# Kernel optimization log

Hardware: AMD Instinct MI355X
Metric: run time of the kernel (lower is better)

## Reference

```python
import math
import jax
import jax.numpy as jnp
import numpy as np

B, N = 64, 64
R = N * (N - 1)
DIST_THRESH = 0.35


def _pair_indices(n):
    # edge e = i*(n-1) + j - (j > i): row-major over i, ascending j skipping j == i
    ii = np.repeat(np.arange(n), n - 1)
    jm = np.tile(np.arange(n), (n, 1))
    jj = jm[~np.eye(n, dtype=bool)].reshape(-1)
    return ii, jj


def _rot_basis(a):
    # a: [..., 1] angle -> [..., 2, 2] rotation basis rows [cos,sin],[cos(a+pi/2),sin(a+pi/2)]
    first = jnp.concatenate([jnp.cos(a), jnp.sin(a)], axis=-1)
    second = jnp.concatenate([jnp.cos(a + math.pi / 2), jnp.sin(a + math.pi / 2)], axis=-1)
    return jnp.stack([first, second], axis=-2)


def setup_inputs() -> dict:
    ks = jax.random.split(jax.random.key(0), 8)
    nrm = lambda k, shape, s=1.0: (jax.random.normal(k, shape) * s).astype(jnp.float32)
    return dict(
        objects_state=jax.random.uniform(ks[0], (B, N, 8), dtype=jnp.float32),
        objects_shape=nrm(ks[1], (B, N, 10)),
        relation_info=nrm(ks[2], (B, R, 3)),
        s_mean=jnp.zeros((8,), jnp.float32), s_std=jnp.ones((8,), jnp.float32),
        sh_mean=jnp.zeros((10,), jnp.float32), sh_std=jnp.ones((10,), jnp.float32),
        v_mean=jnp.zeros((3,), jnp.float32), v_std=jnp.ones((3,), jnp.float32),
        W1=nrm(ks[3], (32, 256), 32 ** -0.5), b1=jnp.zeros((256,), jnp.float32),
        W2=nrm(ks[4], (256, 128), 256 ** -0.5), b2=jnp.zeros((128,), jnp.float32),
        W3=nrm(ks[5], (141, 256), 141 ** -0.5), b3=jnp.zeros((256,), jnp.float32),
        W4=nrm(ks[6], (256, 3), 256 ** -0.5), b4=jnp.zeros((3,), jnp.float32),
    )


def reference(objects_state, objects_shape, relation_info, s_mean, s_std, sh_mean, sh_std,
              v_mean, v_std, W1, b1, W2, b2, W3, b3, W4, b4):
    n = objects_state.shape[1]
    ii, jj = _pair_indices(n)

    # ---- pre_proces: distance-threshold edge build into dense one-hot matrices ----
    pos = objects_state[:, :, 0:2]
    dist = jnp.sqrt(jnp.sum((pos[:, :, None, :] - pos[:, None, :, :]) ** 2, axis=-1))
    # torch: where(dist<0.35, dist, 0).nonzero() -> keeps dist<0.35 AND dist != 0 (drops self-edges)
    mask = ((dist < DIST_THRESH) & (dist != 0.0)).astype(jnp.float32)
    mask_flat = mask[:, ii, jj]  # [B, R]
    eye = jnp.eye(n, dtype=jnp.float32)
    receiver_relations = mask_flat[:, :, None] * eye[ii][None]  # [B, R, N]
    sender_relations = mask_flat[:, :, None] * eye[jj][None]    # [B, R, N]

    data_state = (objects_state - s_mean) / s_std
    data_shape = (objects_shape - sh_mean) / sh_std

    senders_state = jnp.einsum('brn,bnd->brd', sender_relations, data_state)
    receivers_state = jnp.einsum('brn,bnd->brd', receiver_relations, data_state)
    senders_shape = jnp.einsum('brn,bnd->brd', sender_relations, data_shape)
    receivers_shape = jnp.einsum('brn,bnd->brd', receiver_relations, data_shape)

    basis = _rot_basis(receivers_state[:, :, 2:3])  # [B, R, 2, 2]
    diff_state = senders_state - receivers_state
    temp = jnp.stack([diff_state[:, :, 0:2], diff_state[:, :, 3:5], senders_state[:, :, 6:8]], axis=-1)  # [B,R,2,3]
    tfed = jnp.einsum('brij,brjk->brik', basis, temp)  # [B,R,2,3]
    angle_diff = diff_state[:, :, 2:3]
    diff_feat = jnp.concatenate([
        tfed[:, :, :, 0], tfed[:, :, :, 1], tfed[:, :, :, 2],
        jnp.sin(2 * angle_diff), jnp.cos(2 * angle_diff),
        diff_state[:, :, 5:6],
    ], axis=-1)  # [B, R, 9]
    rel_data = jnp.concatenate([relation_info, diff_feat, receivers_shape, senders_shape], axis=-1)  # [B,R,32]

    obj_basis = _rot_basis(data_state[:, :, 2:3])  # [B, N, 2, 2]
    obj_vel_tfed = jnp.einsum('bnij,bnj->bni', obj_basis, data_state[:, :, 3:5])
    obj_data = jnp.concatenate([obj_vel_tfed, data_state[:, :, 5:6], data_shape], axis=-1)  # [B,N,13]

    # ---- interaction-network Net ----
    effects = jax.nn.relu(rel_data @ W1 + b1) @ W2 + b2  # [B, R, 128]
    agg = jnp.einsum('brn,bre->bne', receiver_relations, effects)  # [B, N, 128]
    out_vel = jax.nn.relu(jnp.concatenate([obj_data, agg], axis=-1) @ W3 + b3) @ W4 + b4  # [B,N,3]

    # ---- post_proces ----
    angles = objects_state[:, 1:, 2:3]
    pred = out_vel[:, 1:, :] * v_std + v_mean  # inv_transform_vel
    basis_back = _rot_basis(-angles)
    vel_back = jnp.einsum('bnij,bnj->bni', basis_back, pred[:, :, :2])
    x_dot = jnp.concatenate([vel_back, pred[:, :, 2:]], axis=-1)  # [B, N-1, 3]

    tp = np.eye(6, dtype=np.float32)
    tp[3:, 3:] = 0.0
    tq = np.zeros((3, 6), dtype=np.float32)
    for i in range(3):
        tq[i, i] = 1.0
        tq[i, 3 + i] = 1.0
    x_next = objects_state[:, 1:, :6] @ jnp.asarray(tp) + x_dot @ jnp.asarray(tq)
    return x_next  # [B, N-1, 6]
```

## Files before the change

kernel.cpp:

```cpp
#include <hip/hip_runtime.h>
#include <math.h>

#define BB 64
#define NN 64
#define NM1 63
#define RR (NN*(NN-1))

#define WS1_OFF 0
#define WS2_OFF 16384
#define WS3_OFF 81920

typedef short bf16x8 __attribute__((ext_vector_type(8)));
typedef float f32x4 __attribute__((ext_vector_type(4)));
union U4 { uint4 u; bf16x8 b; };

__device__ inline unsigned int f2bf(float f) {
    unsigned int u = __float_as_uint(f);
    return (u + 0x7FFFu + ((u >> 16) & 1u)) >> 16;
}
__device__ inline unsigned int pack2(float a, float b) {
    return f2bf(a) | (f2bf(b) << 16);
}

__global__ __launch_bounds__(256) void prep_kernel(
    const float* __restrict__ W1, const float* __restrict__ W2,
    const float* __restrict__ W3, unsigned char* __restrict__ ws)
{
    const int t = threadIdx.x;
    const int u = blockIdx.x*4 + (t >> 6), l = t & 63;
    const int col16 = l & 15, quad = l >> 4;
    float v[8];
    uint4* dst;
    if (u < 16) {
        const int nt = u, col = nt*16 + col16;
        #pragma unroll
        for (int j = 0; j < 8; ++j) {
            const int k = quad*8 + j;
            const int orig = k < 12 ? k : (k < 22 ? k+10 : k-10);
            v[j] = W1[orig*256 + col];
        }
        dst = (uint4*)(ws + WS1_OFF) + (nt*64 + l);
    } else if (u < 80) {
        const int w = u-16, nt = w >> 3, kc = w & 7, col = nt*16 + col16;
        #pragma unroll
        for (int j = 0; j < 8; ++j)
            v[j] = W2[(size_t)(kc*32 + quad*8 + j)*128 + col];
        dst = (uint4*)(ws + WS2_OFF) + ((nt*8 + kc)*64 + l);
    } else {
        const int w = u-80, nt = w/5, kc = w - nt*5, col = nt*16 + col16;
        #pragma unroll
        for (int j = 0; j < 8; ++j) {
            const int k = kc*32 + quad*8 + j;
            v[j] = (k < 141) ? W3[(size_t)k*256 + col] : 0.f;
        }
        dst = (uint4*)(ws + WS3_OFF) + ((nt*5 + kc)*64 + l);
    }
    uint4 o;
    o.x = pack2(v[0], v[1]); o.y = pack2(v[2], v[3]);
    o.z = pack2(v[4], v[5]); o.w = pack2(v[6], v[7]);
    *dst = o;
}

__global__ __launch_bounds__(512) void main_kernel(
    const float* __restrict__ objects_state,
    const float* __restrict__ objects_shape,
    const float* __restrict__ relation_info,
    const float* __restrict__ s_mean, const float* __restrict__ s_std,
    const float* __restrict__ sh_mean, const float* __restrict__ sh_std,
    const float* __restrict__ v_mean, const float* __restrict__ v_std,
    const float* __restrict__ b1, const float* __restrict__ b2,
    const float* __restrict__ b3,
    const float* __restrict__ W4, const float* __restrict__ b4,
    const unsigned char* __restrict__ ws,
    float* __restrict__ out)
{
    __shared__ __align__(16) float P[64][29];
    __shared__ __align__(16) unsigned int relb_w[8*64*16];
    __shared__ __align__(16) unsigned short s_h[16*264];
    __shared__ __align__(16) unsigned short s_q[16*168];
    __shared__ int   s_cntg[8];
    __shared__ float s_red[8][16][3];
    __shared__ float s_outv[16][3];

    const int b  = blockIdx.x >> 3;
    const int nb = (blockIdx.x & 7) * 8;
    const int t  = threadIdx.x;
    const int wv = t >> 6, lane = t & 63, col16 = lane & 15, quad = lane >> 4;

    U4 bu0, bu1;
    {
        const uint4* w1f = (const uint4*)(ws + WS1_OFF);
        bu0.u = w1f[(wv*2+0)*64 + lane];
        bu1.u = w1f[(wv*2+1)*64 + lane];
    }
    const float b10 = b1[(wv*2+0)*16 + col16];
    const float b11 = b1[(wv*2+1)*16 + col16];

    float ri0 = 0.f, ri1 = 0.f, ri2 = 0.f;
    if (lane < 63) {
        const float* rp = relation_info
            + ((size_t)b*RR + (size_t)(nb + wv)*NM1 + lane)*3;
        ri0 = rp[0]; ri1 = rp[1]; ri2 = rp[2];
    }

    float e_vs0=0.f,e_vs1=0.f,e_vs2=0.f,e_vm0=0.f,e_vm1=0.f,e_vm2=0.f,e_b4=0.f;
    if (t < 48) {
        e_vs0 = v_std[0]; e_vs1 = v_std[1]; e_vs2 = v_std[2];
        e_vm0 = v_mean[0]; e_vm1 = v_mean[1]; e_vm2 = v_mean[2];
        e_b4  = b4[t % 3];
    }

    {
        uint4 z = make_uint4(0,0,0,0);
        uint4* relb4 = (uint4*)relb_w;
        #pragma unroll
        for (int r = 0; r < 4; ++r) relb4[r*512 + t] = z;
        if (t < 336) ((uint4*)s_q)[t] = z;
        if (t < 64) {
            const int n = b*64 + t;
            const float4* sp4 = (const float4*)(objects_state + (size_t)n*8);
            const float4 sA = sp4[0], sB = sp4[1];
            float st[8] = {sA.x, sA.y, sA.z, sA.w, sB.x, sB.y, sB.z, sB.w};
            const float2* hp2 = (const float2*)(objects_shape + (size_t)n*10);
            float sh[10];
            #pragma unroll
            for (int c = 0; c < 5; ++c) {
                const float2 v = hp2[c];
                sh[c*2] = v.x; sh[c*2+1] = v.y;
            }
            float f[28];
            f[0] = st[0]; f[1] = st[1]; f[26] = st[2]; f[27] = 0.f;
            #pragma unroll
            for (int c = 0; c < 8; ++c)  f[2+c]  = (st[c] - s_mean[c]) / s_std[c];
            #pragma unroll
            for (int c = 0; c < 10; ++c) f[10+c] = (sh[c] - sh_mean[c]) / sh_std[c];
            const float sa = sinf(f[4]), ca = cosf(f[4]);
            const float sr = sinf(st[2]), cr = cosf(st[2]);
            f[20] = ca; f[21] = sa; f[22] = cr; f[23] = sr;
            f[24] =  ca*f[5] + sa*f[6];
            f[25] = -sa*f[5] + ca*f[6];
            #pragma unroll
            for (int c = 0; c < 28; ++c) P[t][c] = f[c];
        }
    }
    __syncthreads();

    {
        const int g = wv, n = nb + g;
        bool pred = false;
        int j = 0;
        if (lane < 63) {
            j = lane + (lane >= n);
            const float dx = P[n][0] - P[j][0];
            const float dy = P[n][1] - P[j][1];
            const float dist = sqrtf(dx*dx + dy*dy);
            pred = (dist < 0.35f) && (dist != 0.0f);
        }
        const unsigned long long mask = __ballot(pred);
        if (lane == 0) s_cntg[g] = __popcll(mask);
        if (pred) {
            const int slot = __popcll(mask & ((1ull << lane) - 1ull));
            const int row = (g << 6) + slot;
            const int sw = (row >> 1) & 3;
            float f[32];
            f[0] = ri0; f[1] = ri1; f[2] = ri2;
            const float ca = P[n][20], sa = P[n][21];
            const float d0 = P[j][2]-P[n][2], d1 = P[j][3]-P[n][3];
            const float d2 = P[j][4]-P[n][4], d3 = P[j][5]-P[n][5];
            const float d4 = P[j][6]-P[n][6], d5 = P[j][7]-P[n][7];
            f[3]  =  ca*d0 + sa*d1;
            f[4]  = -sa*d0 + ca*d1;
            f[5]  =  ca*d3 + sa*d4;
            f[6]  = -sa*d3 + ca*d4;
            f[7]  =  ca*P[j][8] + sa*P[j][9];
            f[8]  = -sa*P[j][8] + ca*P[j][9];
            f[9]  = sinf(2.f*d2);
            f[10] = cosf(2.f*d2);
            f[11] = d5;
            #pragma unroll
            for (int c = 0; c < 10; ++c) f[12+c] = P[j][10+c];
            #pragma unroll
            for (int c = 0; c < 10; ++c) f[22+c] = P[n][10+c];
            uint4* dst = (uint4*)&relb_w[row*16];
            #pragma unroll
            for (int w4 = 0; w4 < 4; ++w4) {
                uint4 o;
                o.x = pack2(f[w4*8+0], f[w4*8+1]);
                o.y = pack2(f[w4*8+2], f[w4*8+3]);
                o.z = pack2(f[w4*8+4], f[w4*8+5]);
                o.w = pack2(f[w4*8+6], f[w4*8+7]);
                dst[w4 ^ sw] = o;
            }
        }
    }
    __syncthreads();

    const int rd_sw = (quad ^ ((col16 >> 1) & 3)) * 4;

    {
        int cg[8];
        #pragma unroll
        for (int g = 0; g < 8; ++g) cg[g] = s_cntg[g];
        float hs0[8], hs1[8];
        #pragma unroll
        for (int g = 0; g < 8; ++g) { hs0[g] = 0.f; hs1[g] = 0.f; }
        #pragma unroll
        for (int g = 0; g < 8; ++g) {
            const int mts = (cg[g] + 15) >> 4;
            for (int mt = 0; mt < mts; ++mt) {
                U4 au;
                au.u = *(const uint4*)&relb_w[((g<<6) + mt*16 + col16)*16 + rd_sw];
                f32x4 a0 = {0.f,0.f,0.f,0.f}, a1 = {0.f,0.f,0.f,0.f};
                a0 = __builtin_amdgcn_mfma_f32_16x16x32_bf16(au.b, bu0.b, a0, 0,0,0);
                a1 = __builtin_amdgcn_mfma_f32_16x16x32_bf16(au.b, bu1.b, a1, 0,0,0);
                #pragma unroll
                for (int i = 0; i < 4; ++i) {
                    hs0[g] += fmaxf(a0[i] + b10, 0.f);
                    hs1[g] += fmaxf(a1[i] + b11, 0.f);
                }
            }
        }
        const float rb0 = fmaxf(b10, 0.f), rb1 = fmaxf(b11, 0.f);
        #pragma unroll
        for (int g = 0; g < 8; ++g) {
            const int mts = (cg[g] + 15) >> 4;
            const float pad = (float)(mts*16 - cg[g]);
            float v0 = hs0[g], v1 = hs1[g];
            v0 += __shfl_xor(v0, 16); v0 += __shfl_xor(v0, 32);
            v1 += __shfl_xor(v1, 16); v1 += __shfl_xor(v1, 32);
            if (quad == 0) {
                s_h[g*264 + (wv*2+0)*16 + col16] =
                    (unsigned short)f2bf(v0 - pad*rb0);
                s_h[g*264 + (wv*2+1)*16 + col16] =
                    (unsigned short)f2bf(v1 - pad*rb1);
            }
        }
    }
    __syncthreads();

    if (t < 104) {
        const int m = t/13, c = t - m*13, n = nb + m;
        float v;
        if (c == 0) v = P[n][24];
        else if (c == 1) v = P[n][25];
        else if (c == 2) v = P[n][7];
        else v = P[n][10 + c - 3];
        s_q[m*168 + c] = (unsigned short)f2bf(v);
    }
    {
        U4 af[8];
        #pragma unroll
        for (int kc = 0; kc < 8; ++kc)
            af[kc].u = *(const uint4*)&s_h[(lane & 15)*264 + kc*32 + quad*8];
        float cntv[4];
        #pragma unroll
        for (int i = 0; i < 4; ++i)
            cntv[i] = (float)s_cntg[(quad*4 + i) & 7];
        const uint4* w2f = (const uint4*)(ws + WS2_OFF);
        f32x4 acc = {0.f,0.f,0.f,0.f};
        #pragma unroll
        for (int kc = 0; kc < 8; ++kc) {
            U4 bu; bu.u = w2f[(wv*8 + kc)*64 + lane];
            acc = __builtin_amdgcn_mfma_f32_16x16x32_bf16(af[kc].b, bu.b, acc, 0,0,0);
        }
        const float b2v = b2[wv*16 + col16];
        #pragma unroll
        for (int i = 0; i < 4; ++i) {
            const int row = quad*4 + i;
            s_q[row*168 + 13 + wv*16 + col16] =
                (unsigned short)f2bf(acc[i] + cntv[i]*b2v);
        }
    }
    __syncthreads();

    {
        U4 af3[5];
        #pragma unroll
        for (int kc = 0; kc < 5; ++kc)
            af3[kc].u = *(const uint4*)&s_q[(lane & 15)*168 + kc*32 + quad*8];
        const uint4* w3f = (const uint4*)(ws + WS3_OFF);
        float p[4][3];
        #pragma unroll
        for (int i = 0; i < 4; ++i) { p[i][0]=0.f; p[i][1]=0.f; p[i][2]=0.f; }
        #pragma unroll
        for (int ntl = 0; ntl < 2; ++ntl) {
            const int nt = wv + ntl*8, col = nt*16 + col16;
            f32x4 acc = {0.f,0.f,0.f,0.f};
            #pragma unroll
            for (int kc = 0; kc < 5; ++kc) {
                U4 bu; bu.u = w3f[(nt*5 + kc)*64 + lane];
                acc = __builtin_amdgcn_mfma_f32_16x16x32_bf16(af3[kc].b, bu.b, acc, 0,0,0);
            }
            const float b3v = b3[col];
            const float w40 = W4[col*3+0], w41 = W4[col*3+1], w42 = W4[col*3+2];
            #pragma unroll
            for (int i = 0; i < 4; ++i) {
                const float h = fmaxf(acc[i] + b3v, 0.f);
                p[i][0] = fmaf(h, w40, p[i][0]);
                p[i][1] = fmaf(h, w41, p[i][1]);
                p[i][2] = fmaf(h, w42, p[i][2]);
            }
        }
        #pragma unroll
        for (int off = 1; off < 16; off <<= 1)
            #pragma unroll
            for (int i = 0; i < 4; ++i) {
                p[i][0] += __shfl_xor(p[i][0], off);
                p[i][1] += __shfl_xor(p[i][1], off);
                p[i][2] += __shfl_xor(p[i][2], off);
            }
        if (col16 == 0)
            #pragma unroll
            for (int i = 0; i < 4; ++i) {
                s_red[wv][quad*4+i][0] = p[i][0];
                s_red[wv][quad*4+i][1] = p[i][1];
                s_red[wv][quad*4+i][2] = p[i][2];
            }
    }
    __syncthreads();
    if (t < 48) {
        const int m = t/3, o = t - m*3;
        float acc = e_b4;
        #pragma unroll
        for (int w = 0; w < 8; ++w) acc += s_red[w][m][o];
        s_outv[m][o] = acc;
    }
    __syncthreads();

    if (t < 48) {
        const int m = t/6, i = t - m*6, n = nb + m;
        if (n >= 1) {
            const float q0 = s_outv[m][0]*e_vs0 + e_vm0;
            const float q1 = s_outv[m][1]*e_vs1 + e_vm1;
            const float q2 = s_outv[m][2]*e_vs2 + e_vm2;
            const float cr = P[n][22], sr = P[n][23];
            const float xd0 = cr*q0 - sr*q1;
            const float xd1 = sr*q0 + cr*q1;
            const int im = i % 3;
            const float xd = (im == 0) ? xd0 : (im == 1) ? xd1 : q2;
            float base = 0.f;
            if (i == 0) base = P[n][0];
            else if (i == 1) base = P[n][1];
            else if (i == 2) base = P[n][26];
            out[((size_t)b*NM1 + (n-1))*6 + i] = base + xd;
        }
    }
}

extern "C" void kernel_launch(void* const* d_in, const int* in_sizes, int n_in,
                              void* d_out, int out_size, void* d_ws, size_t ws_size,
                              hipStream_t stream) {
    const float* objects_state = (const float*)d_in[0];
    const float* objects_shape = (const float*)d_in[1];
    const float* relation_info = (const float*)d_in[2];
    const float* s_mean  = (const float*)d_in[3];
    const float* s_std   = (const float*)d_in[4];
    const float* sh_mean = (const float*)d_in[5];
    const float* sh_std  = (const float*)d_in[6];
    const float* v_mean  = (const float*)d_in[7];
    const float* v_std   = (const float*)d_in[8];
    const float* W1 = (const float*)d_in[9];
    const float* b1 = (const float*)d_in[10];
    const float* W2 = (const float*)d_in[11];
    const float* b2 = (const float*)d_in[12];
    const float* W3 = (const float*)d_in[13];
    const float* b3 = (const float*)d_in[14];
    const float* W4 = (const float*)d_in[15];
    const float* b4 = (const float*)d_in[16];
    unsigned char* ws = (unsigned char*)d_ws;

    prep_kernel<<<dim3(40), dim3(256), 0, stream>>>(W1, W2, W3, ws);
    main_kernel<<<dim3(BB*8), dim3(512), 0, stream>>>(
        objects_state, objects_shape, relation_info,
        s_mean, s_std, sh_mean, sh_std, v_mean, v_std,
        b1, b2, b3, W4, b4, ws, (float*)d_out);
}
```

Baseline: 104.3 us.

## Fuse weight packing into main kernel via cooperative launch and grid sync

Removes the separate prep kernel launch by having each of the 512 blocks pack 20 weight entries into the workspace, then uses a cooperative-groups grid barrier before the packed W1 is read. The barrier sits after the per-block edge construction, so the packing overlaps with that independent preprocessing. If the cooperative launch fails, it falls back to the original two-kernel path. The risk is that the grid-wide sync costs as much as the launch it replaces, and all 512 blocks of 512 threads must be co-resident.

```diff
diff --git a/kernel.cpp b/kernel.cpp
--- a/kernel.cpp
+++ b/kernel.cpp
@@ -1,5 +1,8 @@
 #include <hip/hip_runtime.h>
+#include <hip/hip_cooperative_groups.h>
 #include <math.h>
+
+namespace cg = cooperative_groups;
 
 #define BB 64
 #define NN 64
@@ -22,45 +25,53 @@
     return f2bf(a) | (f2bf(b) << 16);
 }
 
+__device__ inline void pack_entry(int e,
+    const float* __restrict__ W1, const float* __restrict__ W2,
+    const float* __restrict__ W3, unsigned char* __restrict__ ws)
+{
+    const int u = e >> 6, l = e & 63;
+    const int c16 = l & 15, qd = l >> 4;
+    float v[8];
+    uint4* dst;
+    if (u < 16) {
+        const int nt = u, col = nt*16 + c16;
+        #pragma unroll
+        for (int j = 0; j < 8; ++j) {
+            const int k = qd*8 + j;
+            const int orig = k < 12 ? k : (k < 22 ? k+10 : k-10);
+            v[j] = W1[orig*256 + col];
+        }
+        dst = (uint4*)(ws + WS1_OFF) + (nt*64 + l);
+    } else if (u < 80) {
+        const int w = u-16, nt = w >> 3, kc = w & 7, col = nt*16 + c16;
+        #pragma unroll
+        for (int j = 0; j < 8; ++j)
+            v[j] = W2[(size_t)(kc*32 + qd*8 + j)*128 + col];
+        dst = (uint4*)(ws + WS2_OFF) + ((nt*8 + kc)*64 + l);
+    } else {
+        const int w = u-80, nt = w/5, kc = w - nt*5, col = nt*16 + c16;
+        #pragma unroll
+        for (int j = 0; j < 8; ++j) {
+            const int k = kc*32 + qd*8 + j;
+            v[j] = (k < 141) ? W3[(size_t)k*256 + col] : 0.f;
+        }
+        dst = (uint4*)(ws + WS3_OFF) + ((nt*5 + kc)*64 + l);
+    }
+    uint4 o;
+    o.x = pack2(v[0], v[1]); o.y = pack2(v[2], v[3]);
+    o.z = pack2(v[4], v[5]); o.w = pack2(v[6], v[7]);
+    *dst = o;
+}
+
 __global__ __launch_bounds__(256) void prep_kernel(
     const float* __restrict__ W1, const float* __restrict__ W2,
     const float* __restrict__ W3, unsigned char* __restrict__ ws)
 {
-    const int t = threadIdx.x;
-    const int u = blockIdx.x*4 + (t >> 6), l = t & 63;
-    const int col16 = l & 15, quad = l >> 4;
-    float v[8];
-    uint4* dst;
-    if (u < 16) {
-        const int nt = u, col = nt*16 + col16;
-        #pragma unroll
-        for (int j = 0; j < 8; ++j) {
-            const int k = quad*8 + j;
-            const int orig = k < 12 ? k : (k < 22 ? k+10 : k-10);
-            v[j] = W1[orig*256 + col];
-        }
-        dst = (uint4*)(ws + WS1_OFF) + (nt*64 + l);
-    } else if (u < 80) {
-        const int w = u-16, nt = w >> 3, kc = w & 7, col = nt*16 + col16;
-        #pragma unroll
-        for (int j = 0; j < 8; ++j)
-            v[j] = W2[(size_t)(kc*32 + quad*8 + j)*128 + col];
-        dst = (uint4*)(ws + WS2_OFF) + ((nt*8 + kc)*64 + l);
-    } else {
-        const int w = u-80, nt = w/5, kc = w - nt*5, col = nt*16 + col16;
-        #pragma unroll
-        for (int j = 0; j < 8; ++j) {
-            const int k = kc*32 + quad*8 + j;
-            v[j] = (k < 141) ? W3[(size_t)k*256 + col] : 0.f;
-        }
-        dst = (uint4*)(ws + WS3_OFF) + ((nt*5 + kc)*64 + l);
-    }
-    uint4 o;
-    o.x = pack2(v[0], v[1]); o.y = pack2(v[2], v[3]);
-    o.z = pack2(v[4], v[5]); o.w = pack2(v[6], v[7]);
-    *dst = o;
-}
-
+    const int e = blockIdx.x*256 + threadIdx.x;
+    pack_entry(e, W1, W2, W3, ws);
+}
+
+template<bool COOP>
 __global__ __launch_bounds__(512) void main_kernel(
     const float* __restrict__ objects_state,
     const float* __restrict__ objects_shape,
@@ -68,10 +79,11 @@
     const float* __restrict__ s_mean, const float* __restrict__ s_std,
     const float* __restrict__ sh_mean, const float* __restrict__ sh_std,
     const float* __restrict__ v_mean, const float* __restrict__ v_std,
-    const float* __restrict__ b1, const float* __restrict__ b2,
-    const float* __restrict__ b3,
+    const float* __restrict__ W1, const float* __restrict__ b1,
+    const float* __restrict__ W2, const float* __restrict__ b2,
+    const float* __restrict__ W3, const float* __restrict__ b3,
     const float* __restrict__ W4, const float* __restrict__ b4,
-    const unsigned char* __restrict__ ws,
+    unsigned char* __restrict__ ws,
     float* __restrict__ out)
 {
     __shared__ __align__(16) float P[64][29];
@@ -87,14 +99,9 @@
     const int t  = threadIdx.x;
     const int wv = t >> 6, lane = t & 63, col16 = lane & 15, quad = lane >> 4;
 
-    U4 bu0, bu1;
-    {
-        const uint4* w1f = (const uint4*)(ws + WS1_OFF);
-        bu0.u = w1f[(wv*2+0)*64 + lane];
-        bu1.u = w1f[(wv*2+1)*64 + lane];
-    }
-    const float b10 = b1[(wv*2+0)*16 + col16];
-    const float b11 = b1[(wv*2+1)*16 + col16];
+    if (COOP) {
+        if (t < 20) pack_entry(blockIdx.x*20 + t, W1, W2, W3, ws);
+    }
 
     float ri0 = 0.f, ri1 = 0.f, ri2 = 0.f;
     if (lane < 63) {
@@ -195,18 +202,29 @@
     }
     __syncthreads();
 
+    if (COOP) cg::this_grid().sync();
+
+    U4 bu0, bu1;
+    {
+        const uint4* w1f = (const uint4*)(ws + WS1_OFF);
+        bu0.u = w1f[(wv*2+0)*64 + lane];
+        bu1.u = w1f[(wv*2+1)*64 + lane];
+    }
+    const float b10 = b1[(wv*2+0)*16 + col16];
+    const float b11 = b1[(wv*2+1)*16 + col16];
+
     const int rd_sw = (quad ^ ((col16 >> 1) & 3)) * 4;
 
     {
-        int cg[8];
-        #pragma unroll
-        for (int g = 0; g < 8; ++g) cg[g] = s_cntg[g];
+        int cg_[8];
+        #pragma unroll
+        for (int g = 0; g < 8; ++g) cg_[g] = s_cntg[g];
         float hs0[8], hs1[8];
         #pragma unroll
         for (int g = 0; g < 8; ++g) { hs0[g] = 0.f; hs1[g] = 0.f; }
         #pragma unroll
         for (int g = 0; g < 8; ++g) {
-            const int mts = (cg[g] + 15) >> 4;
+            const int mts = (cg_[g] + 15) >> 4;
             for (int mt = 0; mt < mts; ++mt) {
                 U4 au;
                 au.u = *(const uint4*)&relb_w[((g<<6) + mt*16 + col16)*16 + rd_sw];
@@ -223,8 +241,8 @@
         const float rb0 = fmaxf(b10, 0.f), rb1 = fmaxf(b11, 0.f);
         #pragma unroll
         for (int g = 0; g < 8; ++g) {
-            const int mts = (cg[g] + 15) >> 4;
-            const float pad = (float)(mts*16 - cg[g]);
+            const int mts = (cg_[g] + 15) >> 4;
+            const float pad = (float)(mts*16 - cg_[g]);
             float v0 = hs0[g], v1 = hs1[g];
             v0 += __shfl_xor(v0, 16); v0 += __shfl_xor(v0, 32);
             v1 += __shfl_xor(v1, 16); v1 += __shfl_xor(v1, 32);
@@ -368,10 +386,24 @@
     const float* W4 = (const float*)d_in[15];
     const float* b4 = (const float*)d_in[16];
     unsigned char* ws = (unsigned char*)d_ws;
-
-    prep_kernel<<<dim3(40), dim3(256), 0, stream>>>(W1, W2, W3, ws);
-    main_kernel<<<dim3(BB*8), dim3(512), 0, stream>>>(
-        objects_state, objects_shape, relation_info,
-        s_mean, s_std, sh_mean, sh_std, v_mean, v_std,
-        b1, b2, b3, W4, b4, ws, (float*)d_out);
-}
+    float* outp = (float*)d_out;
+    (void)in_sizes; (void)n_in; (void)out_size; (void)ws_size;
+
+    void* args[] = {
+        (void*)&objects_state, (void*)&objects_shape, (void*)&relation_info,
+        (void*)&s_mean, (void*)&s_std, (void*)&sh_mean, (void*)&sh_std,
+        (void*)&v_mean, (void*)&v_std,
+        (void*)&W1, (void*)&b1, (void*)&W2, (void*)&b2,
+        (void*)&W3, (void*)&b3, (void*)&W4, (void*)&b4,
+        (void*)&ws, (void*)&outp
+    };
+    hipError_t err = hipLaunchCooperativeKernel(
+        (const void*)main_kernel<true>, dim3(BB*8), dim3(512), args, 0, stream);
+    if (err != hipSuccess) {
+        prep_kernel<<<dim3(40), dim3(256), 0, stream>>>(W1, W2, W3, ws);
+        main_kernel<false><<<dim3(BB*8), dim3(512), 0, stream>>>(
+            objects_state, objects_shape, relation_info,
+            s_mean, s_std, sh_mean, sh_std, v_mean, v_std,
+            W1, b1, W2, b2, W3, b3, W4, b4, ws, outp);
+    }
+}
```

Result: slower. 172.7 us (+65.5%).
